# Optimization experiments

Hardware: AMD Instinct MI355X
Metric: run time of the kernel (lower is better)

Reference implementation:

```python
import jax, jax.numpy as jnp
import numpy as np

N, E, EMB, HID, FT, H = 2000, 32000, 768, 384, 768, 4
NEG_SLOPE = 0.2


def gat_conv(x, src, dst, edge_attr, W, a_src, a_dst, W_e, a_e, b):
    """PyG GATConv, concat=False (mean over heads), edge_dim, add_self_loops
    with fill_value='mean'. x:[N,Fin], edge_attr:[E,768]."""
    n = x.shape[0]
    h, c = a_src.shape
    # self loops: edge_attr of loop (i,i) = mean of incoming edge_attr at i
    deg = jax.ops.segment_sum(jnp.ones(src.shape[0], x.dtype), dst, num_segments=n)
    loop_attr = jax.ops.segment_sum(edge_attr, dst, num_segments=n) / jnp.maximum(deg, 1.0)[:, None]
    ar = jnp.arange(n)
    s = jnp.concatenate([src, ar])
    d = jnp.concatenate([dst, ar])
    ea = jnp.concatenate([edge_attr, loop_attr], axis=0)   # [E+N, 768]
    hx = (x @ W).reshape(n, h, c)                           # [N,H,C]
    he = (ea @ W_e).reshape(-1, h, c)                       # [E+N,H,C]
    alpha = (jnp.einsum('nhc,hc->nh', hx, a_src)[s]
             + jnp.einsum('nhc,hc->nh', hx, a_dst)[d]
             + jnp.einsum('ehc,hc->eh', he, a_e))           # [E+N,H]
    alpha = jax.nn.leaky_relu(alpha, NEG_SLOPE)
    # segment softmax over destination node (self loop guarantees nonempty)
    mx = jax.ops.segment_max(alpha, d, num_segments=n)
    ex = jnp.exp(alpha - mx[d])
    den = jax.ops.segment_sum(ex, d, num_segments=n)
    att = ex / den[d]                                       # [E+N,H]
    out = jax.ops.segment_sum(hx[s] * att[:, :, None], d, num_segments=n)  # [N,H,C]
    return out.mean(axis=1) + b


def setup_inputs() -> dict:
    key = jax.random.key(0)
    ks = jax.random.split(key, 16)
    w = lambda k, shape, s=0.05: (jax.random.normal(k, shape, jnp.float32) * s)
    return {
        'x': jax.random.randint(ks[0], (N, 2), 0, 178),
        'edge_index': jax.random.randint(ks[1], (2, E), 0, N),
        'edge_attr': jax.random.randint(ks[2], (E, 2), 0, 18),
        'x_emb': w(ks[3], (178, EMB)),
        'e_emb': w(ks[4], (18, EMB)),
        'W1': w(ks[5], (EMB, H * HID)),
        'as1': w(ks[6], (H, HID)),
        'ad1': w(ks[7], (H, HID)),
        'We1': w(ks[8], (EMB, H * HID)),
        'ae1': w(ks[9], (H, HID)),
        'b1': jnp.zeros((HID,), jnp.float32),
        'W2': w(ks[10], (HID, H * FT)),
        'as2': w(ks[11], (H, FT)),
        'ad2': w(ks[12], (H, FT)),
        'We2': w(ks[13], (EMB, H * FT)),
        'ae2': w(ks[14], (H, FT)),
        'b2': jnp.zeros((FT,), jnp.float32),
    }


def reference(x, edge_index, edge_attr, x_emb, e_emb, W1, as1, ad1, We1, ae1, b1,
              W2, as2, ad2, We2, ae2, b2):
    src, dst = edge_index[0], edge_index[1]
    xf = x_emb[x].sum(axis=1)          # [N,768]
    eaf = e_emb[edge_attr].sum(axis=1)  # [E,768]
    h = jax.nn.relu(gat_conv(xf, src, dst, eaf, W1, as1, ad1, We1, ae1, b1))
    out = gat_conv(h, src, dst, eaf, W2, as2, ad2, We2, ae2, b2)
    return out
```

## Files before the change

kernel.cpp:

```cpp
#include <hip/hip_runtime.h>
#include <hip/hip_bf16.h>

#define NN   2000
#define NE   32000
#define EMBD 768
#define NH   4
#define HID  384
#define NEG  0.2f
#define DCAP 128

#define GM 2000
#define GN 768
#define GK 1536
#define K1 768

typedef __bf16 bf16x8 __attribute__((ext_vector_type(8)));
typedef float  f32x4  __attribute__((ext_vector_type(4)));

__device__ inline float wsum(float v){
#pragma unroll
  for (int o = 32; o > 0; o >>= 1) v += __shfl_xor(v, o, 64);
  return v;
}
__device__ inline float wmax(float v){
#pragma unroll
  for (int o = 32; o > 0; o >>= 1) v = fmaxf(v, __shfl_xor(v, o, 64));
  return v;
}

__device__ inline unsigned short f2bf(float f){
  unsigned u = __float_as_uint(f);
  unsigned r = (u + 0x7FFFu + ((u >> 16) & 1u)) >> 16;
  return (unsigned short)r;
}
__device__ inline float bf2f(unsigned short h){
  return __uint_as_float(((unsigned)h) << 16);
}

__device__ inline void gload16(const void* g, void* l){
  __builtin_amdgcn_global_load_lds((const __attribute__((address_space(1))) void*)g,
                                   (__attribute__((address_space(3))) void*)l, 16, 0, 0);
}
__device__ inline float dot4(float4 a, float4 b){
  return a.x*b.x + a.y*b.y + a.z*b.z + a.w*b.w;
}

__global__ __launch_bounds__(1024) void k_cnt(const int* __restrict__ dst,
                                              int* __restrict__ offsets,
                                              int* __restrict__ cursor){
  __shared__ int cnt[NN];
  __shared__ int s[1024];
  int t = threadIdx.x;
  for (int i = t; i < NN; i += 1024) cnt[i] = 0;
  __syncthreads();
  for (int e = t; e < NE; e += 1024) atomicAdd(&cnt[dst[e]], 1);
  __syncthreads();
  int a = (2*t   < NN) ? cnt[2*t  ] : 0;
  int b = (2*t+1 < NN) ? cnt[2*t+1] : 0;
  s[t] = a + b;
  __syncthreads();
  for (int off = 1; off < 1024; off <<= 1){
    int v = (t >= off) ? s[t-off] : 0;
    __syncthreads();
    s[t] += v;
    __syncthreads();
  }
  int base = (t > 0) ? s[t-1] : 0;
  if (2*t < NN){ offsets[2*t] = base; cursor[2*t] = base; }
  if (2*t+1 < NN){ offsets[2*t+1] = base + a; cursor[2*t+1] = base + a; }
  if (2*t == NN) offsets[NN] = base;
}

__global__ __launch_bounds__(256) void k_prepA(
    const float* __restrict__ We1, const float* __restrict__ ae1,
    const float* __restrict__ W2,  const float* __restrict__ as2,
    const float* __restrict__ ad2, const float* __restrict__ We2,
    const float* __restrict__ ae2, const float* __restrict__ W1,
    const float* __restrict__ x_emb, const int* __restrict__ dst,
    float* __restrict__ we_a1, float* __restrict__ wa_s2,
    float* __restrict__ wa_d2, float* __restrict__ we_a2,
    unsigned short* __restrict__ Bh, unsigned short* __restrict__ Bl,
    unsigned short* __restrict__ W1th, unsigned short* __restrict__ W1tl,
    unsigned short* __restrict__ Xeh, unsigned short* __restrict__ Xel,
    int* __restrict__ cursor, int* __restrict__ csr){
  __shared__ __align__(16) float tile[64][65];
  int blk = blockIdx.x, t = threadIdx.x;
  if (blk < 384){
    int wid = blk*4 + (t >> 6);
    int lane = t & 63;
    bool lo32 = lane < 32;
    if (wid < 384){
      int kg = wid >> 2, h = wid & 3;
      int k0 = kg*8;
      const float4* ap = (const float4*)(ae1 + h*384);
      float4 a0 = ap[lane];
      float4 a1 = lo32 ? ap[64+lane] : make_float4(0,0,0,0);
      float res[8];
#pragma unroll
      for (int r = 0; r < 8; ++r){
        const float4* wr = (const float4*)(We1 + (size_t)(k0+r)*1536 + h*384);
        float s = dot4(wr[lane], a0);
        if (lo32) s += dot4(wr[64+lane], a1);
        res[r] = s;
      }
#pragma unroll
      for (int r = 0; r < 8; ++r) res[r] = wsum(res[r]);
      if (lane == 0){
#pragma unroll
        for (int r = 0; r < 8; ++r) we_a1[(k0+r)*4+h] = res[r];
      }
    } else if (wid < 768){
      int t2 = wid - 384;
      int kg = t2 >> 2, h = t2 & 3;
      int k0 = kg*4;
      const float4* s4 = (const float4*)(as2 + h*768);
      const float4* d4 = (const float4*)(ad2 + h*768);
      float4 sa[3], da[3];
#pragma unroll
      for (int i = 0; i < 3; ++i){ sa[i] = s4[i*64+lane]; da[i] = d4[i*64+lane]; }
      float r1[4], r2[4];
#pragma unroll
      for (int r = 0; r < 4; ++r){
        const float4* wr = (const float4*)(W2 + (size_t)(k0+r)*3072 + h*768);
        float s1 = 0.f, s2 = 0.f;
#pragma unroll
        for (int i = 0; i < 3; ++i){
          float4 w = wr[i*64+lane];
          s1 += dot4(w, sa[i]); s2 += dot4(w, da[i]);
        }
        r1[r] = s1; r2[r] = s2;
      }
#pragma unroll
      for (int r = 0; r < 4; ++r){ r1[r] = wsum(r1[r]); r2[r] = wsum(r2[r]); }
      if (lane == 0){
#pragma unroll
        for (int r = 0; r < 4; ++r){ wa_s2[(k0+r)*4+h] = r1[r]; wa_d2[(k0+r)*4+h] = r2[r]; }
      }
    } else {
      int t2 = wid - 768;
      int kg = t2 >> 2, h = t2 & 3;
      int k0 = kg*4;
      const float4* ap = (const float4*)(ae2 + h*768);
      float4 aa[3];
#pragma unroll
      for (int i = 0; i < 3; ++i) aa[i] = ap[i*64+lane];
      float res[4];
#pragma unroll
      for (int r = 0; r < 4; ++r){
        const float4* wr = (const float4*)(We2 + (size_t)(k0+r)*3072 + h*768);
        float s = 0.f;
#pragma unroll
        for (int i = 0; i < 3; ++i) s += dot4(wr[i*64+lane], aa[i]);
        res[r] = s;
      }
#pragma unroll
      for (int r = 0; r < 4; ++r) res[r] = wsum(res[r]);
      if (lane == 0){
#pragma unroll
        for (int r = 0; r < 4; ++r) we_a2[(k0+r)*4+h] = res[r];
      }
    }
  } else if (blk < 672){
    int idx = blk - 384;
    int bk = (idx % 24) * 64;
    int bc = (idx / 24) * 64;
    int cc = t & 63, kk4 = t >> 6;
#pragma unroll
    for (int i = 0; i < 16; ++i){
      int kk = kk4*16 + i;
      int k = bk + kk;
      int h = k / 384, kp = k - h*384;
      tile[kk][cc] = W2[(size_t)kp*3072 + h*768 + bc + cc];
    }
    __syncthreads();
    int kk2 = t & 63, cc4 = t >> 6;
#pragma unroll
    for (int i = 0; i < 16; ++i){
      int c2 = cc4*16 + i;
      float v = tile[kk2][c2];
      unsigned short hi = f2bf(v);
      unsigned short lo = f2bf(v - bf2f(hi));
      size_t o = (size_t)(bc + c2)*GK + bk + kk2;
      Bh[o] = hi; Bl[o] = lo;
    }
  } else if (blk < 960){
    int idx = blk - 672;
    int bkk = (idx % 12) * 64;
    int bcc = (idx / 12) * 64;
    int cc = t & 63, kk4 = t >> 6;
#pragma unroll
    for (int i = 0; i < 16; ++i){
      int kk = kk4*16 + i;
      tile[kk][cc] = W1[(size_t)(bkk+kk)*1536 + bcc + cc];
    }
    __syncthreads();
    int kk2 = t & 63, cc4 = t >> 6;
#pragma unroll
    for (int i = 0; i < 16; ++i){
      int c2 = cc4*16 + i;
      float v = tile[kk2][c2];
      unsigned short hi = f2bf(v);
      unsigned short lo = f2bf(v - bf2f(hi));
      size_t o = (size_t)(bcc + c2)*768 + bkk + kk2;
      W1th[o] = hi; W1tl[o] = lo;
    }
  } else if (blk < 1094){
    int i = (blk - 960)*256 + t;
    if (i < 34176){
      float4 v = ((const float4*)x_emb)[i];
      unsigned short h0 = f2bf(v.x), h1 = f2bf(v.y), h2 = f2bf(v.z), h3 = f2bf(v.w);
      ushort4 hh; hh.x = h0; hh.y = h1; hh.z = h2; hh.w = h3;
      ushort4 ll; ll.x = f2bf(v.x - bf2f(h0)); ll.y = f2bf(v.y - bf2f(h1));
      ll.z = f2bf(v.z - bf2f(h2)); ll.w = f2bf(v.w - bf2f(h3));
      ((ushort4*)Xeh)[i] = hh;
      ((ushort4*)Xel)[i] = ll;
    }
  } else {
    int e = (blk - 1094)*256 + t;
    if (e < NE){
      int pz = atomicAdd(&cursor[dst[e]], 1);
      csr[pz] = e;
    }
  }
}

__global__ __launch_bounds__(256) void k_mmX(const unsigned short* __restrict__ Ah,
                                             const unsigned short* __restrict__ Al,
                                             const unsigned short* __restrict__ Bh,
                                             const unsigned short* __restrict__ Bl,
                                             float* __restrict__ xh1){
  __shared__ __align__(16) unsigned short lds[2][4][64][64];
  int b = blockIdx.x;
  int bm = b / 24, bn = b % 24;
  int wave = threadIdx.x >> 6, lane = threadIdx.x & 63;
  int wm = wave >> 1, wn = wave & 1;
  int rl = lane & 15, kq = lane >> 4;

  int rt   = lane >> 3;
  int kswz = ((lane & 7) ^ rt) * 8;
  const unsigned short* sbase;
  int rowbase;
  if (wave == 0){ sbase = Ah; rowbase = bm*64; }
  else if (wave == 1){ sbase = Al; rowbase = bm*64; }
  else if (wave == 2){ sbase = Bh; rowbase = bn*64; }
  else { sbase = Bl; rowbase = bn*64; }
  bool isA = wave < 2;

  f32x4 acc[2][2] = {};

#pragma unroll
  for (int i = 0; i < 8; ++i){
    int row = rowbase + i*8 + rt;
    if (isA) row = (row < 178) ? row : 177;
    gload16(sbase + (size_t)row*768 + kswz, &lds[0][wave][i*8][0]);
  }
  __syncthreads();

  for (int t = 0; t < 12; ++t){
    int cur = t & 1;
    if (t < 11){
      int k0 = (t+1)*64;
#pragma unroll
      for (int i = 0; i < 8; ++i){
        int row = rowbase + i*8 + rt;
        if (isA) row = (row < 178) ? row : 177;
        gload16(sbase + (size_t)row*768 + k0 + kswz, &lds[cur^1][wave][i*8][0]);
      }
    }
#pragma unroll
    for (int ks = 0; ks < 2; ++ks){
      bf16x8 ah[2], al2[2], bh2[2], bl2[2];
#pragma unroll
      for (int i = 0; i < 2; ++i){
        int r = wm*32 + i*16 + rl;
        int sl = (ks*4 + kq) ^ (r & 7);
        ah[i]  = *(const bf16x8*)&lds[cur][0][r][sl*8];
        al2[i] = *(const bf16x8*)&lds[cur][1][r][sl*8];
      }
#pragma unroll
      for (int j = 0; j < 2; ++j){
        int cdx = wn*32 + j*16 + rl;
        int sl = (ks*4 + kq) ^ (cdx & 7);
        bh2[j] = *(const bf16x8*)&lds[cur][2][cdx][sl*8];
        bl2[j] = *(const bf16x8*)&lds[cur][3][cdx][sl*8];
      }
#pragma unroll
      for (int i = 0; i < 2; ++i){
#pragma unroll
        for (int j = 0; j < 2; ++j){
          acc[i][j] = __builtin_amdgcn_mfma_f32_16x16x32_bf16(ah[i],  bh2[j], acc[i][j], 0, 0, 0);
          acc[i][j] = __builtin_amdgcn_mfma_f32_16x16x32_bf16(ah[i],  bl2[j], acc[i][j], 0, 0, 0);
          acc[i][j] = __builtin_amdgcn_mfma_f32_16x16x32_bf16(al2[i], bh2[j], acc[i][j], 0, 0, 0);
        }
      }
    }
    __syncthreads();
  }

#pragma unroll
  for (int i = 0; i < 2; ++i){
#pragma unroll
    for (int j = 0; j < 2; ++j){
      int col = bn*64 + wn*32 + j*16 + rl;
#pragma unroll
      for (int r = 0; r < 4; ++r){
        int row = bm*64 + wm*32 + i*16 + kq*4 + r;
        if (row < 178) xh1[(size_t)row*1536 + col] = acc[i][j][r];
      }
    }
  }
}

__global__ __launch_bounds__(256) void k_prepB(
    const float* __restrict__ xh1,
    const float* __restrict__ as1, const float* __restrict__ ad1,
    const float* __restrict__ e_emb,
    const float* __restrict__ we_a1, const float* __restrict__ we_a2,
    unsigned short* __restrict__ XHh, unsigned short* __restrict__ XHl,
    float* __restrict__ xa_s1, float* __restrict__ xa_d1,
    float* __restrict__ ew1, float* __restrict__ ew2){
  int blk = blockIdx.x, t = threadIdx.x;
  if (blk < 178){
    int tok = blk;
    for (int i = t; i < 1536; i += 256){
      float v = xh1[(size_t)tok*1536 + i];
      int h = i / 384, c = i - h*384;
      size_t off = (size_t)c*K1 + h*192 + tok;
      unsigned short hi = f2bf(v);
      XHh[off] = hi; XHl[off] = f2bf(v - bf2f(hi));
    }
  } else if (blk < 356){
    int r = blk - 178;
    int h = t >> 6, lane = t & 63;
    const float4* p0 = (const float4*)(xh1 + (size_t)r*1536 + h*384);
    const float4* s4 = (const float4*)(as1 + h*384);
    const float4* d4 = (const float4*)(ad1 + h*384);
    float s1, s2;
    {
      float4 u = p0[lane], sa = s4[lane], da = d4[lane];
      s1 = dot4(u, sa); s2 = dot4(u, da);
    }
    if (lane < 32){
      float4 u = p0[64+lane], sa = s4[64+lane], da = d4[64+lane];
      s1 += dot4(u, sa); s2 += dot4(u, da);
    }
    s1 = wsum(s1); s2 = wsum(s2);
    if (lane == 0){ xa_s1[r*4+h] = s1; xa_d1[r*4+h] = s2; }
  } else if (blk < 392){
    int id = (blk - 356)*4 + (t >> 6);
    int lane = t & 63;
    const float* wv = (id < 72) ? we_a1 : we_a2;
    float* o = (id < 72) ? ew1 : ew2;
    int id2 = (id < 72) ? id : (id - 72);
    int r = id2 >> 2, h = id2 & 3;
    const float* ar = e_emb + (size_t)r*EMBD;
    float acc = 0.f;
    for (int k = lane; k < EMBD; k += 64) acc += ar[k] * wv[k*4+h];
    acc = wsum(acc);
    if (lane == 0) o[r*4+h] = acc;
  } else {
    int i = (blk - 392)*256 + t;
    if (i < 21504){
      int c = i / 56, rem = i - c*56;
      int h = rem / 14, tp = 178 + rem - h*14;
      size_t off = (size_t)c*K1 + h*192 + tp;
      XHh[off] = 0; XHl[off] = 0;
    }
  }
}

__global__ __launch_bounds__(256) void k_gat1sm(const int* __restrict__ offsets,
                      int* __restrict__ csr, const int* __restrict__ srcv,
                      const int* __restrict__ x, const int* __restrict__ ea,
                      const float* __restrict__ xa_s1, const float* __restrict__ xa_d1,
                      const float* __restrict__ ew1, float* __restrict__ spill,
                      unsigned short* __restrict__ Qh, unsigned short* __restrict__ Ql){
  __shared__ float wts[DCAP][5];
  __shared__ int   sE[DCAP];
  __shared__ int   sA[DCAP], sB[DCAP];
  __shared__ float coef[K1];
  int n = blockIdx.x, t = threadIdx.x;
  int w = t >> 6, lane = t & 63;
  int lo = offsets[n], hi = offsets[n+1];
  int deg = hi - lo;
  bool big = deg > DCAP;

  if (!big){
    if (deg <= 64){
      if (w == 0){
        int v = (lane < deg) ? csr[lo+lane] : 0x7fffffff;
#pragma unroll
        for (int k = 2; k <= 64; k <<= 1){
#pragma unroll
          for (int j2 = k >> 1; j2 > 0; j2 >>= 1){
            int o = __shfl_xor(v, j2, 64);
            bool lower = (lane & j2) == 0;
            bool asc   = (lane & k) == 0;
            v = (lower == asc) ? min(v, o) : max(v, o);
          }
        }
        sE[lane] = v;
        if (lane < deg) csr[lo+lane] = v;
      }
    } else {
      int m = 1; while (m < deg) m <<= 1;
      for (int i = t; i < m; i += 256) sE[i] = (i < deg) ? csr[lo+i] : 0x7fffffff;
      __syncthreads();
      for (int k = 2; k <= m; k <<= 1){
        for (int j2 = k >> 1; j2 > 0; j2 >>= 1){
          for (int i = t; i < m; i += 256){
            int ixj = i ^ j2;
            if (ixj > i){
              int a = sE[i], b = sE[ixj];
              bool up = ((i & k) == 0);
              if ((a > b) == up){ sE[i] = b; sE[ixj] = a; }
            }
          }
          __syncthreads();
        }
      }
      for (int i = t; i < deg; i += 256) csr[lo+i] = sE[i];
    }
  } else {
    if (t == 0){
      for (int i = lo+1; i < hi; ++i){
        int v = csr[i], j = i-1;
        while (j >= lo && csr[j] > v){ csr[j+1] = csr[j]; --j; }
        csr[j+1] = v;
      }
    }
  }
  for (int i = t; i < K1; i += 256) coef[i] = 0.f;
  __syncthreads();

  int xn0 = x[2*n], xn1 = x[2*n+1];
  float ad_n = xa_d1[xn0*4+w] + xa_d1[xn1*4+w];
  float as_n = xa_s1[xn0*4+w] + xa_s1[xn1*4+w];
  float mx = -3.4e38f, sae = 0.f;
  float wlv;
  if (!big){
    for (int j = lane; j < deg; j += 64){
      int e = sE[j]; int s = srcv[e];
      int a = x[2*s], b = x[2*s+1];
      if (w == 0){ sA[j] = a; sB[j] = b; }
      float ae = ew1[ea[2*e]*4+w] + ew1[ea[2*e+1]*4+w];
      float al = (xa_s1[a*4+w] + xa_s1[b*4+w]) + ad_n + ae;
      al = (al > 0.f) ? al : NEG * al;
      wts[j][w] = al;
      sae += ae; mx = fmaxf(mx, al);
    }
    mx = wmax(mx); sae = wsum(sae);
    float all_ = as_n + ad_n + sae / fmaxf((float)deg, 1.f);
    all_ = (all_ > 0.f) ? all_ : NEG * all_;
    mx = fmaxf(mx, all_);
    float den = 0.f;
    for (int j = lane; j < deg; j += 64){
      float xx = expf(wts[j][w] - mx);
      wts[j][w] = xx; den += xx;
    }
    den = wsum(den);
    float exl = expf(all_ - mx);
    den += exl;
    float inv = 1.f / den;
    for (int j = lane; j < deg; j += 64) wts[j][w] *= inv;
    wlv = exl * inv;
  } else {
    for (int p = lo + lane; p < hi; p += 64){
      int e = csr[p]; int s = srcv[e];
      int a = x[2*s], b = x[2*s+1];
      float ae = ew1[ea[2*e]*4+w] + ew1[ea[2*e+1]*4+w];
      float al = (xa_s1[a*4+w] + xa_s1[b*4+w]) + ad_n + ae;
      al = (al > 0.f) ? al : NEG * al;
      spill[e*4 + w] = al;
      sae += ae; mx = fmaxf(mx, al);
    }
    mx = wmax(mx); sae = wsum(sae);
    float all_ = as_n + ad_n + sae / fmaxf((float)deg, 1.f);
    all_ = (all_ > 0.f) ? all_ : NEG * all_;
    mx = fmaxf(mx, all_);
    float den = 0.f;
    for (int p = lo + lane; p < hi; p += 64){
      int e = csr[p];
      float xx = expf(spill[e*4 + w] - mx);
      spill[e*4 + w] = xx; den += xx;
    }
    den = wsum(den);
    float exl = expf(all_ - mx);
    den += exl;
    float inv = 1.f / den;
    for (int p = lo + lane; p < hi; p += 64) spill[csr[p]*4 + w] *= inv;
    wlv = exl * inv;
  }
  __syncthreads();

  if (lane == 0){
    float* cf = coef + w*192;
    if (!big){
      for (int j = 0; j < deg; ++j){
        float wj = wts[j][w];
        cf[sA[j]] += wj; cf[sB[j]] += wj;
      }
    } else {
      for (int p = lo; p < hi; ++p){
        int e = csr[p]; int s = srcv[e];
        float wj = spill[e*4 + w];
        cf[x[2*s]] += wj; cf[x[2*s+1]] += wj;
      }
    }
    cf[xn0] += wlv; cf[xn1] += wlv;
  }
  __syncthreads();

  for (int i = t; i < K1; i += 256){
    float v = coef[i];
    unsigned short hi16 = f2bf(v);
    Qh[(size_t)n*K1 + i] = hi16;
    Ql[(size_t)n*K1 + i] = f2bf(v - bf2f(hi16));
  }
}

__global__ __launch_bounds__(256) void k_mm1(const unsigned short* __restrict__ Qh,
                                             const unsigned short* __restrict__ Ql,
                                             const unsigned short* __restrict__ XHh,
                                             const unsigned short* __restrict__ XHl,
                                             const float* __restrict__ b1,
                                             float* __restrict__ hact){
  __shared__ __align__(16) unsigned short lds[2][4][64][64];
  int b = blockIdx.x;
  int xcd = b & 7, idx = b >> 3;
  int bm = xcd*4 + idx/6, bn = idx % 6;
  int wave = threadIdx.x >> 6, lane = threadIdx.x & 63;
  int wm = wave >> 1, wn = wave & 1;
  int rl = lane & 15, kq = lane >> 4;

  int rt   = lane >> 3;
  int kswz = ((lane & 7) ^ rt) * 8;
  const unsigned short* sbase;
  int rowbase;
  if (wave == 0){ sbase = Qh; rowbase = bm*64; }
  else if (wave == 1){ sbase = Ql; rowbase = bm*64; }
  else if (wave == 2){ sbase = XHh; rowbase = bn*64; }
  else { sbase = XHl; rowbase = bn*64; }
  bool isA = wave < 2;

  f32x4 acc[2][2] = {};

#pragma unroll
  for (int i = 0; i < 8; ++i){
    int row = rowbase + i*8 + rt;
    if (isA) row = (row < GM) ? row : (GM-1);
    gload16(sbase + (size_t)row*K1 + kswz, &lds[0][wave][i*8][0]);
  }
  __syncthreads();

  for (int t = 0; t < 12; ++t){
    int cur = t & 1;
    if (t < 11){
      int k0 = (t+1)*64;
#pragma unroll
      for (int i = 0; i < 8; ++i){
        int row = rowbase + i*8 + rt;
        if (isA) row = (row < GM) ? row : (GM-1);
        gload16(sbase + (size_t)row*K1 + k0 + kswz, &lds[cur^1][wave][i*8][0]);
      }
    }
#pragma unroll
    for (int ks = 0; ks < 2; ++ks){
      bf16x8 ah[2], al2[2], bh2[2], bl2[2];
#pragma unroll
      for (int i = 0; i < 2; ++i){
        int r = wm*32 + i*16 + rl;
        int sl = (ks*4 + kq) ^ (r & 7);
        ah[i]  = *(const bf16x8*)&lds[cur][0][r][sl*8];
        al2[i] = *(const bf16x8*)&lds[cur][1][r][sl*8];
      }
#pragma unroll
      for (int j = 0; j < 2; ++j){
        int cdx = wn*32 + j*16 + rl;
        int sl = (ks*4 + kq) ^ (cdx & 7);
        bh2[j] = *(const bf16x8*)&lds[cur][2][cdx][sl*8];
        bl2[j] = *(const bf16x8*)&lds[cur][3][cdx][sl*8];
      }
#pragma unroll
      for (int i = 0; i < 2; ++i){
#pragma unroll
        for (int j = 0; j < 2; ++j){
          acc[i][j] = __builtin_amdgcn_mfma_f32_16x16x32_bf16(ah[i],  bh2[j], acc[i][j], 0, 0, 0);
          acc[i][j] = __builtin_amdgcn_mfma_f32_16x16x32_bf16(ah[i],  bl2[j], acc[i][j], 0, 0, 0);
          acc[i][j] = __builtin_amdgcn_mfma_f32_16x16x32_bf16(al2[i], bh2[j], acc[i][j], 0, 0, 0);
        }
      }
    }
    __syncthreads();
  }

#pragma unroll
  for (int i = 0; i < 2; ++i){
#pragma unroll
    for (int j = 0; j < 2; ++j){
      int col = bn*64 + wn*32 + j*16 + rl;
      float bb = b1[col];
#pragma unroll
      for (int r = 0; r < 4; ++r){
        int row = bm*64 + wm*32 + i*16 + kq*4 + r;
        if (row < GM) hact[(size_t)row*HID + col] = fmaxf(0.25f*acc[i][j][r] + bb, 0.f);
      }
    }
  }
}

__global__ __launch_bounds__(256) void k_dots(const float* __restrict__ hact,
                      const float* __restrict__ wa_s2, const float* __restrict__ wa_d2,
                      float* __restrict__ asrc2, float* __restrict__ adst2){
  int w = threadIdx.x >> 6, lane = threadIdx.x & 63;
  int n = blockIdx.x*4 + w;
  float pr[8] = {};
#pragma unroll
  for (int i = 0; i < 6; ++i){
    int c = i*64 + lane;
    float v = hact[(size_t)n*HID + c];
#pragma unroll
    for (int h = 0; h < 4; ++h){
      pr[h]   += v * wa_s2[c*4+h];
      pr[4+h] += v * wa_d2[c*4+h];
    }
  }
#pragma unroll
  for (int o = 32; o > 0; o >>= 1){
#pragma unroll
    for (int q = 0; q < 8; ++q) pr[q] += __shfl_xor(pr[q], o, 64);
  }
  if (lane == 0){
#pragma unroll
    for (int h = 0; h < 4; ++h){ asrc2[n*4+h] = pr[h]; adst2[n*4+h] = pr[4+h]; }
  }
}

__global__ __launch_bounds__(384) void k_gat2(const int* __restrict__ offsets,
                      const int* __restrict__ csr, const int* __restrict__ srcv,
                      const int* __restrict__ ea,
                      const float* __restrict__ asrc, const float* __restrict__ adst,
                      const float* __restrict__ ew2,
                      const float* __restrict__ hact, float* __restrict__ spill,
                      unsigned short* __restrict__ Gh, unsigned short* __restrict__ Gl){
  __shared__ float wts[DCAP][5];
  __shared__ int   ssrc[DCAP];
  __shared__ float wl[4];
  int n = blockIdx.x, t = threadIdx.x;
  int w = t >> 6, lane = t & 63;
  int lo = offsets[n], hi = offsets[n+1];
  int deg = hi - lo;
  bool big = deg > DCAP;
  if (w < 4){
    float ad_n = adst[n*NH + w];
    float as_n = asrc[n*NH + w];
    float mx = -3.4e38f, sae = 0.f;
    if (!big){
      for (int p = lo + lane; p < hi; p += 64){
        int e = csr[p]; int s = srcv[e];
        if (w == 0) ssrc[p - lo] = s;
        float ae = ew2[ea[2*e]*4+w] + ew2[ea[2*e+1]*4+w];
        float al = asrc[s*NH + w] + ad_n + ae;
        al = (al > 0.f) ? al : NEG * al;
        wts[p - lo][w] = al;
        sae += ae; mx = fmaxf(mx, al);
      }
      mx = wmax(mx); sae = wsum(sae);
      float all_ = as_n + ad_n + sae / fmaxf((float)deg, 1.f);
      all_ = (all_ > 0.f) ? all_ : NEG * all_;
      mx = fmaxf(mx, all_);
      float den = 0.f;
      for (int p = lo + lane; p < hi; p += 64){
        float xx = expf(wts[p - lo][w] - mx);
        wts[p - lo][w] = xx; den += xx;
      }
      den = wsum(den);
      float exl = expf(all_ - mx);
      den += exl;
      float inv = 1.f / den;
      for (int p = lo + lane; p < hi; p += 64) wts[p - lo][w] *= inv;
      if (lane == 0) wl[w] = exl * inv;
    } else {
      for (int p = lo + lane; p < hi; p += 64){
        int e = csr[p];
        float ae = ew2[ea[2*e]*4+w] + ew2[ea[2*e+1]*4+w];
        float al = asrc[srcv[e]*NH + w] + ad_n + ae;
        al = (al > 0.f) ? al : NEG * al;
        spill[e*4 + w] = al;
        sae += ae; mx = fmaxf(mx, al);
      }
      mx = wmax(mx); sae = wsum(sae);
      float all_ = as_n + ad_n + sae / fmaxf((float)deg, 1.f);
      all_ = (all_ > 0.f) ? all_ : NEG * all_;
      mx = fmaxf(mx, all_);
      float den = 0.f;
      for (int p = lo + lane; p < hi; p += 64){
        int e = csr[p];
        float xx = expf(spill[e*4 + w] - mx);
        spill[e*4 + w] = xx; den += xx;
      }
      den = wsum(den);
      float exl = expf(all_ - mx);
      den += exl;
      float inv = 1.f / den;
      for (int p = lo + lane; p < hi; p += 64) spill[csr[p]*4 + w] *= inv;
      if (lane == 0) wl[w] = exl * inv;
    }
  }
  __syncthreads();

  int c = t;
  float a0 = 0.f, a1 = 0.f, a2 = 0.f, a3 = 0.f;
  if (!big){
    float vnext = 0.f;
    if (deg > 0) vnext = hact[(size_t)ssrc[0]*HID + c];
    for (int j = 0; j < deg; ++j){
      float vc = vnext;
      if (j+1 < deg) vnext = hact[(size_t)ssrc[j+1]*HID + c];
      float w0=wts[j][0], w1=wts[j][1], w2=wts[j][2], w3=wts[j][3];
      a0 += w0*vc; a1 += w1*vc; a2 += w2*vc; a3 += w3*vc;
    }
  } else {
    for (int j = 0; j < deg; ++j){
      int e = csr[lo+j]; int s = srcv[e];
      float w0 = spill[e*4+0], w1 = spill[e*4+1], w2 = spill[e*4+2], w3 = spill[e*4+3];
      float vc = hact[(size_t)s*HID + c];
      a0 += w0*vc; a1 += w1*vc; a2 += w2*vc; a3 += w3*vc;
    }
  }
  {
    float vc = hact[(size_t)n*HID + c];
    a0 += wl[0]*vc; a1 += wl[1]*vc; a2 += wl[2]*vc; a3 += wl[3]*vc;
  }
  size_t base = (size_t)n*GK + c;
  float vv[4] = {a0, a1, a2, a3};
#pragma unroll
  for (int h = 0; h < 4; ++h){
    unsigned short hi16 = f2bf(vv[h]);
    unsigned short lo16 = f2bf(vv[h] - bf2f(hi16));
    Gh[base + h*384] = hi16;
    Gl[base + h*384] = lo16;
  }
}

__global__ __launch_bounds__(256) void k_mm2(const unsigned short* __restrict__ Gh,
                                             const unsigned short* __restrict__ Gl,
                                             const unsigned short* __restrict__ Bh,
                                             const unsigned short* __restrict__ Bl,
                                             const float* __restrict__ b2,
                                             float* __restrict__ out){
  __shared__ __align__(16) unsigned short lds[2][4][64][64];
  int b = blockIdx.x;
  int xcd = b & 7, idx = b >> 3;
  int bm = xcd*4 + idx/12, bn = idx % 12;
  int wave = threadIdx.x >> 6, lane = threadIdx.x & 63;
  int wm = wave >> 1, wn = wave & 1;
  int rl = lane & 15, kq = lane >> 4;

  int rt   = lane >> 3;
  int kswz = ((lane & 7) ^ rt) * 8;
  const unsigned short* sbase;
  int rowbase;
  if (wave == 0){ sbase = Gh; rowbase = bm*64; }
  else if (wave == 1){ sbase = Gl; rowbase = bm*64; }
  else if (wave == 2){ sbase = Bh; rowbase = bn*64; }
  else { sbase = Bl; rowbase = bn*64; }
  bool isA = wave < 2;

  f32x4 acc[2][2] = {};

#pragma unroll
  for (int i = 0; i < 8; ++i){
    int row = rowbase + i*8 + rt;
    if (isA) row = (row < GM) ? row : (GM-1);
    gload16(sbase + (size_t)row*GK + kswz, &lds[0][wave][i*8][0]);
  }
  __syncthreads();

  for (int t = 0; t < 24; ++t){
    int cur = t & 1;
    if (t < 23){
      int k0 = (t+1)*64;
#pragma unroll
      for (int i = 0; i < 8; ++i){
        int row = rowbase + i*8 + rt;
        if (isA) row = (row < GM) ? row : (GM-1);
        gload16(sbase + (size_t)row*GK + k0 + kswz, &lds[cur^1][wave][i*8][0]);
      }
    }
#pragma unroll
    for (int ks = 0; ks < 2; ++ks){
      bf16x8 ah[2], al2[2], bh2[2], bl2[2];
#pragma unroll
      for (int i = 0; i < 2; ++i){
        int r = wm*32 + i*16 + rl;
        int sl = (ks*4 + kq) ^ (r & 7);
        ah[i]  = *(const bf16x8*)&lds[cur][0][r][sl*8];
        al2[i] = *(const bf16x8*)&lds[cur][1][r][sl*8];
      }
#pragma unroll
      for (int j = 0; j < 2; ++j){
        int cdx = wn*32 + j*16 + rl;
        int sl = (ks*4 + kq) ^ (cdx & 7);
        bh2[j] = *(const bf16x8*)&lds[cur][2][cdx][sl*8];
        bl2[j] = *(const bf16x8*)&lds[cur][3][cdx][sl*8];
      }
#pragma unroll
      for (int i = 0; i < 2; ++i){
#pragma unroll
        for (int j = 0; j < 2; ++j){
          acc[i][j] = __builtin_amdgcn_mfma_f32_16x16x32_bf16(ah[i],  bh2[j], acc[i][j], 0, 0, 0);
          acc[i][j] = __builtin_amdgcn_mfma_f32_16x16x32_bf16(ah[i],  bl2[j], acc[i][j], 0, 0, 0);
          acc[i][j] = __builtin_amdgcn_mfma_f32_16x16x32_bf16(al2[i], bh2[j], acc[i][j], 0, 0, 0);
        }
      }
    }
    __syncthreads();
  }

#pragma unroll
  for (int i = 0; i < 2; ++i){
#pragma unroll
    for (int j = 0; j < 2; ++j){
      int col = bn*64 + wn*32 + j*16 + rl;
      float bb = b2[col];
#pragma unroll
      for (int r = 0; r < 4; ++r){
        int row = bm*64 + wm*32 + i*16 + kq*4 + r;
        if (row < GM) out[(size_t)row*GN + col] = 0.25f*acc[i][j][r] + bb;
      }
    }
  }
}

extern "C" void kernel_launch(void* const* d_in, const int* in_sizes, int n_in,
                              void* d_out, int out_size, void* d_ws, size_t ws_size,
                              hipStream_t stream){
  const int*   x     = (const int*)d_in[0];
  const int*   ei    = (const int*)d_in[1];
  const int*   ea    = (const int*)d_in[2];
  const float* x_emb = (const float*)d_in[3];
  const float* e_emb = (const float*)d_in[4];
  const float* W1    = (const float*)d_in[5];
  const float* as1   = (const float*)d_in[6];
  const float* ad1   = (const float*)d_in[7];
  const float* We1   = (const float*)d_in[8];
  const float* ae1   = (const float*)d_in[9];
  const float* b1    = (const float*)d_in[10];
  const float* W2    = (const float*)d_in[11];
  const float* as2   = (const float*)d_in[12];
  const float* ad2   = (const float*)d_in[13];
  const float* We2   = (const float*)d_in[14];
  const float* ae2   = (const float*)d_in[15];
  const float* b2    = (const float*)d_in[16];
  const int* srcv = ei;
  const int* dstv = ei + NE;
  float* out = (float*)d_out;

  char* p = (char*)d_ws;
  auto take = [&](size_t n){ void* q = (void*)p; p += (n + 255) & ~(size_t)255; return q; };
  int*   cursor  = (int*)take(NN*4);
  int*   offsets = (int*)take((NN+1)*4);
  int*   csr     = (int*)take(NE*4);
  float* we_a1   = (float*)take(EMBD*NH*4);
  float* wa_s2   = (float*)take(HID*NH*4);
  float* wa_d2   = (float*)take(HID*NH*4);
  float* we_a2   = (float*)take(EMBD*NH*4);
  float* xa_s1   = (float*)take(178*NH*4);
  float* xa_d1   = (float*)take(178*NH*4);
  float* ew1     = (float*)take(18*NH*4);
  float* ew2     = (float*)take(18*NH*4);
  float* xh1     = (float*)take((size_t)178*1536*4);
  unsigned short* Xeh  = (unsigned short*)take((size_t)178*768*2);
  unsigned short* Xel  = (unsigned short*)take((size_t)178*768*2);
  unsigned short* W1th = (unsigned short*)take((size_t)1536*768*2);
  unsigned short* W1tl = (unsigned short*)take((size_t)1536*768*2);
  unsigned short* XHh  = (unsigned short*)take((size_t)HID*K1*2);
  unsigned short* XHl  = (unsigned short*)take((size_t)HID*K1*2);
  unsigned short* Qh   = (unsigned short*)take((size_t)NN*K1*2);
  unsigned short* Ql   = (unsigned short*)take((size_t)NN*K1*2);
  unsigned short* Bth  = (unsigned short*)take((size_t)GN*GK*2);
  unsigned short* Btl  = (unsigned short*)take((size_t)GN*GK*2);
  unsigned short* Gh   = (unsigned short*)take((size_t)GM*GK*2);
  unsigned short* Gl   = (unsigned short*)take((size_t)GM*GK*2);
  float* spill   = (float*)take((size_t)NE*NH*4);
  float* hact    = (float*)take((size_t)NN*HID*4);
  float* asrc2   = (float*)take(NN*NH*4);
  float* adst2   = (float*)take(NN*NH*4);

  k_cnt<<<1, 1024, 0, stream>>>(dstv, offsets, cursor);

  k_prepA<<<1219, 256, 0, stream>>>(We1, ae1, W2, as2, ad2, We2, ae2, W1,
                                    x_emb, dstv, we_a1, wa_s2, wa_d2, we_a2,
                                    Bth, Btl, W1th, W1tl, Xeh, Xel,
                                    cursor, csr);
  k_mmX<<<72, 256, 0, stream>>>(Xeh, Xel, W1th, W1tl, xh1);
  k_prepB<<<476, 256, 0, stream>>>(xh1, as1, ad1, e_emb, we_a1, we_a2,
                                   XHh, XHl, xa_s1, xa_d1, ew1, ew2);

  k_gat1sm<<<NN, 256, 0, stream>>>(offsets, csr, srcv, x, ea, xa_s1, xa_d1,
                                   ew1, spill, Qh, Ql);
  k_mm1<<<192, 256, 0, stream>>>(Qh, Ql, XHh, XHl, b1, hact);
  k_dots<<<500, 256, 0, stream>>>(hact, wa_s2, wa_d2, asrc2, adst2);

  k_gat2<<<NN, 384, 0, stream>>>(offsets, csr, srcv, ea, asrc2, adst2, ew2,
                                 hact, spill, Gh, Gl);

  k_mm2<<<384, 256, 0, stream>>>(Gh, Gl, Bth, Btl, b2, out);
}
```

Baseline: 117.0 us.

## Fold prepB into mmX by precomputing W1·a_src/a_dst and writing split bf16 directly

Precomputes W1 projected onto the layer-1 attention vectors (wa_s1, wa_d1) in the prep kernel, so per-token attention logits come straight from x_emb instead of from the intermediate xh1. The x_emb-by-W1 GEMM now writes the hi/lo bf16 transposed XH layout in its epilogue, and the zero-padding and edge-embedding dot work moves into the prep and mmX launches. This drops the fp32 xh1 buffer and one kernel launch with its global round trip. The reassociation changes the fp32 rounding order of the attention logits slightly.

```diff
diff --git a/kernel.cpp b/kernel.cpp
--- a/kernel.cpp
+++ b/kernel.cpp
@@ -76,12 +76,15 @@
     const float* __restrict__ W2,  const float* __restrict__ as2,
     const float* __restrict__ ad2, const float* __restrict__ We2,
     const float* __restrict__ ae2, const float* __restrict__ W1,
+    const float* __restrict__ as1, const float* __restrict__ ad1,
     const float* __restrict__ x_emb, const int* __restrict__ dst,
     float* __restrict__ we_a1, float* __restrict__ wa_s2,
     float* __restrict__ wa_d2, float* __restrict__ we_a2,
+    float* __restrict__ wa_s1, float* __restrict__ wa_d1,
     unsigned short* __restrict__ Bh, unsigned short* __restrict__ Bl,
     unsigned short* __restrict__ W1th, unsigned short* __restrict__ W1tl,
     unsigned short* __restrict__ Xeh, unsigned short* __restrict__ Xel,
+    unsigned short* __restrict__ XHh, unsigned short* __restrict__ XHl,
     int* __restrict__ cursor, int* __restrict__ csr){
   __shared__ __align__(16) float tile[64][65];
   int blk = blockIdx.x, t = threadIdx.x;
@@ -160,8 +163,42 @@
         for (int r = 0; r < 4; ++r) we_a2[(k0+r)*4+h] = res[r];
       }
     }
-  } else if (blk < 672){
-    int idx = blk - 384;
+  } else if (blk < 480){
+    int wid = (blk-384)*4 + (t >> 6);
+    int lane = t & 63;
+    bool lo32 = lane < 32;
+    int kg = wid >> 2, h = wid & 3;
+    int k0 = kg*8;
+    const float4* sp = (const float4*)(as1 + h*384);
+    const float4* dp = (const float4*)(ad1 + h*384);
+    float4 sa0 = sp[lane];
+    float4 sa1 = lo32 ? sp[64+lane] : make_float4(0,0,0,0);
+    float4 da0 = dp[lane];
+    float4 da1 = lo32 ? dp[64+lane] : make_float4(0,0,0,0);
+    float r1[8], r2[8];
+#pragma unroll
+    for (int r = 0; r < 8; ++r){
+      const float4* wr = (const float4*)(W1 + (size_t)(k0+r)*1536 + h*384);
+      float4 w0 = wr[lane];
+      float s1 = dot4(w0, sa0);
+      float s2 = dot4(w0, da0);
+      if (lo32){
+        float4 w1 = wr[64+lane];
+        s1 += dot4(w1, sa1); s2 += dot4(w1, da1);
+      }
+      r1[r] = s1; r2[r] = s2;
+    }
+#pragma unroll
+    for (int r = 0; r < 8; ++r){ r1[r] = wsum(r1[r]); r2[r] = wsum(r2[r]); }
+    if (lane == 0){
+#pragma unroll
+      for (int r = 0; r < 8; ++r){
+        wa_s1[h*768 + k0 + r] = r1[r];
+        wa_d1[h*768 + k0 + r] = r2[r];
+      }
+    }
+  } else if (blk < 768){
+    int idx = blk - 480;
     int bk = (idx % 24) * 64;
     int bc = (idx / 24) * 64;
     int cc = t & 63, kk4 = t >> 6;
@@ -183,8 +220,8 @@
       size_t o = (size_t)(bc + c2)*GK + bk + kk2;
       Bh[o] = hi; Bl[o] = lo;
     }
-  } else if (blk < 960){
-    int idx = blk - 672;
+  } else if (blk < 1056){
+    int idx = blk - 768;
     int bkk = (idx % 12) * 64;
     int bcc = (idx / 12) * 64;
     int cc = t & 63, kk4 = t >> 6;
@@ -204,8 +241,8 @@
       size_t o = (size_t)(bcc + c2)*768 + bkk + kk2;
       W1th[o] = hi; W1tl[o] = lo;
     }
-  } else if (blk < 1094){
-    int i = (blk - 960)*256 + t;
+  } else if (blk < 1190){
+    int i = (blk - 1056)*256 + t;
     if (i < 34176){
       float4 v = ((const float4*)x_emb)[i];
       unsigned short h0 = f2bf(v.x), h1 = f2bf(v.y), h2 = f2bf(v.z), h3 = f2bf(v.w);
@@ -215,8 +252,16 @@
       ((ushort4*)Xeh)[i] = hh;
       ((ushort4*)Xel)[i] = ll;
     }
+  } else if (blk < 1274){
+    int i = (blk - 1190)*256 + t;
+    if (i < 21504){
+      int c = i / 56, rem = i - c*56;
+      int h = rem / 14, tp = 178 + rem - h*14;
+      size_t off = (size_t)c*K1 + h*192 + tp;
+      XHh[off] = 0; XHl[off] = 0;
+    }
   } else {
-    int e = (blk - 1094)*256 + t;
+    int e = (blk - 1274)*256 + t;
     if (e < NE){
       int pz = atomicAdd(&cursor[dst[e]], 1);
       csr[pz] = e;
@@ -228,127 +273,125 @@
                                              const unsigned short* __restrict__ Al,
                                              const unsigned short* __restrict__ Bh,
                                              const unsigned short* __restrict__ Bl,
-                                             float* __restrict__ xh1){
+                                             const float* __restrict__ x_emb,
+                                             const float* __restrict__ e_emb,
+                                             const float* __restrict__ wa_s1,
+                                             const float* __restrict__ wa_d1,
+                                             const float* __restrict__ we_a1,
+                                             const float* __restrict__ we_a2,
+                                             unsigned short* __restrict__ XHh,
+                                             unsigned short* __restrict__ XHl,
+                                             float* __restrict__ xa_s1,
+                                             float* __restrict__ xa_d1,
+                                             float* __restrict__ ew1,
+                                             float* __restrict__ ew2){
   __shared__ __align__(16) unsigned short lds[2][4][64][64];
-  int b = blockIdx.x;
-  int bm = b / 24, bn = b % 24;
-  int wave = threadIdx.x >> 6, lane = threadIdx.x & 63;
-  int wm = wave >> 1, wn = wave & 1;
-  int rl = lane & 15, kq = lane >> 4;
-
-  int rt   = lane >> 3;
-  int kswz = ((lane & 7) ^ rt) * 8;
-  const unsigned short* sbase;
-  int rowbase;
-  if (wave == 0){ sbase = Ah; rowbase = bm*64; }
-  else if (wave == 1){ sbase = Al; rowbase = bm*64; }
-  else if (wave == 2){ sbase = Bh; rowbase = bn*64; }
-  else { sbase = Bl; rowbase = bn*64; }
-  bool isA = wave < 2;
-
-  f32x4 acc[2][2] = {};
-
-#pragma unroll
-  for (int i = 0; i < 8; ++i){
-    int row = rowbase + i*8 + rt;
-    if (isA) row = (row < 178) ? row : 177;
-    gload16(sbase + (size_t)row*768 + kswz, &lds[0][wave][i*8][0]);
-  }
-  __syncthreads();
-
-  for (int t = 0; t < 12; ++t){
-    int cur = t & 1;
-    if (t < 11){
-      int k0 = (t+1)*64;
-#pragma unroll
-      for (int i = 0; i < 8; ++i){
-        int row = rowbase + i*8 + rt;
-        if (isA) row = (row < 178) ? row : 177;
-        gload16(sbase + (size_t)row*768 + k0 + kswz, &lds[cur^1][wave][i*8][0]);
-      }
-    }
-#pragma unroll
-    for (int ks = 0; ks < 2; ++ks){
-      bf16x8 ah[2], al2[2], bh2[2], bl2[2];
-#pragma unroll
-      for (int i = 0; i < 2; ++i){
-        int r = wm*32 + i*16 + rl;
-        int sl = (ks*4 + kq) ^ (r & 7);
-        ah[i]  = *(const bf16x8*)&lds[cur][0][r][sl*8];
-        al2[i] = *(const bf16x8*)&lds[cur][1][r][sl*8];
-      }
+  int blk = blockIdx.x;
+  if (blk < 72){
+    int b = blk;
+    int bm = b / 24, bn = b % 24;
+    int wave = threadIdx.x >> 6, lane = threadIdx.x & 63;
+    int wm = wave >> 1, wn = wave & 1;
+    int rl = lane & 15, kq = lane >> 4;
+
+    int rt   = lane >> 3;
+    int kswz = ((lane & 7) ^ rt) * 8;
+    const unsigned short* sbase;
+    int rowbase;
+    if (wave == 0){ sbase = Ah; rowbase = bm*64; }
+    else if (wave == 1){ sbase = Al; rowbase = bm*64; }
+    else if (wave == 2){ sbase = Bh; rowbase = bn*64; }
+    else { sbase = Bl; rowbase = bn*64; }
+    bool isA = wave < 2;
+
+    f32x4 acc[2][2] = {};
+
+#pragma unroll
+    for (int i = 0; i < 8; ++i){
+      int row = rowbase + i*8 + rt;
+      if (isA) row = (row < 178) ? row : 177;
+      gload16(sbase + (size_t)row*768 + kswz, &lds[0][wave][i*8][0]);
+    }
+    __syncthreads();
+
+    for (int t = 0; t < 12; ++t){
+      int cur = t & 1;
+      if (t < 11){
+        int k0 = (t+1)*64;
+#pragma unroll
+        for (int i = 0; i < 8; ++i){
+          int row = rowbase + i*8 + rt;
+          if (isA) row = (row < 178) ? row : 177;
+          gload16(sbase + (size_t)row*768 + k0 + kswz, &lds[cur^1][wave][i*8][0]);
+        }
+      }
+#pragma unroll
+      for (int ks = 0; ks < 2; ++ks){
+        bf16x8 ah[2], al2[2], bh2[2], bl2[2];
+#pragma unroll
+        for (int i = 0; i < 2; ++i){
+          int r = wm*32 + i*16 + rl;
+          int sl = (ks*4 + kq) ^ (r & 7);
+          ah[i]  = *(const bf16x8*)&lds[cur][0][r][sl*8];
+          al2[i] = *(const bf16x8*)&lds[cur][1][r][sl*8];
+        }
+#pragma unroll
+        for (int j = 0; j < 2; ++j){
+          int cdx = wn*32 + j*16 + rl;
+          int sl = (ks*4 + kq) ^ (cdx & 7);
+          bh2[j] = *(const bf16x8*)&lds[cur][2][cdx][sl*8];
+          bl2[j] = *(const bf16x8*)&lds[cur][3][cdx][sl*8];
+        }
+#pragma unroll
+        for (int i = 0; i < 2; ++i){
+#pragma unroll
+          for (int j = 0; j < 2; ++j){
+            acc[i][j] = __builtin_amdgcn_mfma_f32_16x16x32_bf16(ah[i],  bh2[j], acc[i][j], 0, 0, 0);
+            acc[i][j] = __builtin_amdgcn_mfma_f32_16x16x32_bf16(ah[i],  bl2[j], acc[i][j], 0, 0, 0);
+            acc[i][j] = __builtin_amdgcn_mfma_f32_16x16x32_bf16(al2[i], bh2[j], acc[i][j], 0, 0, 0);
+          }
+        }
+      }
+      __syncthreads();
+    }
+
+#pragma unroll
+    for (int i = 0; i < 2; ++i){
 #pragma unroll
       for (int j = 0; j < 2; ++j){
-        int cdx = wn*32 + j*16 + rl;
-        int sl = (ks*4 + kq) ^ (cdx & 7);
-        bh2[j] = *(const bf16x8*)&lds[cur][2][cdx][sl*8];
-        bl2[j] = *(const bf16x8*)&lds[cur][3][cdx][sl*8];
-      }
-#pragma unroll
-      for (int i = 0; i < 2; ++i){
-#pragma unroll
-        for (int j = 0; j < 2; ++j){
-          acc[i][j] = __builtin_amdgcn_mfma_f32_16x16x32_bf16(ah[i],  bh2[j], acc[i][j], 0, 0, 0);
-          acc[i][j] = __builtin_amdgcn_mfma_f32_16x16x32_bf16(ah[i],  bl2[j], acc[i][j], 0, 0, 0);
-          acc[i][j] = __builtin_amdgcn_mfma_f32_16x16x32_bf16(al2[i], bh2[j], acc[i][j], 0, 0, 0);
+        int col = bn*64 + wn*32 + j*16 + rl;
+        int h = col / 384, c = col - h*384;
+        size_t cb = (size_t)c*K1 + h*192;
+#pragma unroll
+        for (int r = 0; r < 4; ++r){
+          int row = bm*64 + wm*32 + i*16 + kq*4 + r;
+          if (row < 178){
+            float v = acc[i][j][r];
+            unsigned short hi = f2bf(v);
+            XHh[cb + row] = hi;
+            XHl[cb + row] = f2bf(v - bf2f(hi));
+          }
         }
       }
     }
-    __syncthreads();
-  }
-
-#pragma unroll
-  for (int i = 0; i < 2; ++i){
-#pragma unroll
-    for (int j = 0; j < 2; ++j){
-      int col = bn*64 + wn*32 + j*16 + rl;
-#pragma unroll
-      for (int r = 0; r < 4; ++r){
-        int row = bm*64 + wm*32 + i*16 + kq*4 + r;
-        if (row < 178) xh1[(size_t)row*1536 + col] = acc[i][j][r];
-      }
-    }
-  }
-}
-
-__global__ __launch_bounds__(256) void k_prepB(
-    const float* __restrict__ xh1,
-    const float* __restrict__ as1, const float* __restrict__ ad1,
-    const float* __restrict__ e_emb,
-    const float* __restrict__ we_a1, const float* __restrict__ we_a2,
-    unsigned short* __restrict__ XHh, unsigned short* __restrict__ XHl,
-    float* __restrict__ xa_s1, float* __restrict__ xa_d1,
-    float* __restrict__ ew1, float* __restrict__ ew2){
-  int blk = blockIdx.x, t = threadIdx.x;
-  if (blk < 178){
-    int tok = blk;
-    for (int i = t; i < 1536; i += 256){
-      float v = xh1[(size_t)tok*1536 + i];
-      int h = i / 384, c = i - h*384;
-      size_t off = (size_t)c*K1 + h*192 + tok;
-      unsigned short hi = f2bf(v);
-      XHh[off] = hi; XHl[off] = f2bf(v - bf2f(hi));
-    }
-  } else if (blk < 356){
-    int r = blk - 178;
-    int h = t >> 6, lane = t & 63;
-    const float4* p0 = (const float4*)(xh1 + (size_t)r*1536 + h*384);
-    const float4* s4 = (const float4*)(as1 + h*384);
-    const float4* d4 = (const float4*)(ad1 + h*384);
-    float s1, s2;
-    {
-      float4 u = p0[lane], sa = s4[lane], da = d4[lane];
-      s1 = dot4(u, sa); s2 = dot4(u, da);
-    }
-    if (lane < 32){
-      float4 u = p0[64+lane], sa = s4[64+lane], da = d4[64+lane];
-      s1 += dot4(u, sa); s2 += dot4(u, da);
+  } else if (blk < 250){
+    int r = blk - 72;
+    int h = threadIdx.x >> 6, lane = threadIdx.x & 63;
+    const float4* xe = (const float4*)(x_emb + (size_t)r*768);
+    const float4* ws = (const float4*)(wa_s1 + h*768);
+    const float4* wd = (const float4*)(wa_d1 + h*768);
+    float s1 = 0.f, s2 = 0.f;
+#pragma unroll
+    for (int i = 0; i < 3; ++i){
+      float4 u = xe[i*64+lane];
+      s1 += dot4(u, ws[i*64+lane]);
+      s2 += dot4(u, wd[i*64+lane]);
     }
     s1 = wsum(s1); s2 = wsum(s2);
     if (lane == 0){ xa_s1[r*4+h] = s1; xa_d1[r*4+h] = s2; }
-  } else if (blk < 392){
-    int id = (blk - 356)*4 + (t >> 6);
-    int lane = t & 63;
+  } else {
+    int id = (blk - 250)*4 + (threadIdx.x >> 6);
+    int lane = threadIdx.x & 63;
     const float* wv = (id < 72) ? we_a1 : we_a2;
     float* o = (id < 72) ? ew1 : ew2;
     int id2 = (id < 72) ? id : (id - 72);
@@ -358,14 +401,6 @@
     for (int k = lane; k < EMBD; k += 64) acc += ar[k] * wv[k*4+h];
     acc = wsum(acc);
     if (lane == 0) o[r*4+h] = acc;
-  } else {
-    int i = (blk - 392)*256 + t;
-    if (i < 21504){
-      int c = i / 56, rem = i - c*56;
-      int h = rem / 14, tp = 178 + rem - h*14;
-      size_t off = (size_t)c*K1 + h*192 + tp;
-      XHh[off] = 0; XHl[off] = 0;
-    }
   }
 }
 
@@ -866,11 +901,12 @@
   float* wa_s2   = (float*)take(HID*NH*4);
   float* wa_d2   = (float*)take(HID*NH*4);
   float* we_a2   = (float*)take(EMBD*NH*4);
+  float* wa_s1   = (float*)take(NH*EMBD*4);
+  float* wa_d1   = (float*)take(NH*EMBD*4);
   float* xa_s1   = (float*)take(178*NH*4);
   float* xa_d1   = (float*)take(178*NH*4);
   float* ew1     = (float*)take(18*NH*4);
   float* ew2     = (float*)take(18*NH*4);
-  float* xh1     = (float*)take((size_t)178*1536*4);
   unsigned short* Xeh  = (unsigned short*)take((size_t)178*768*2);
   unsigned short* Xel  = (unsigned short*)take((size_t)178*768*2);
   unsigned short* W1th = (unsigned short*)take((size_t)1536*768*2);
@@ -890,13 +926,15 @@
 
   k_cnt<<<1, 1024, 0, stream>>>(dstv, offsets, cursor);
 
-  k_prepA<<<1219, 256, 0, stream>>>(We1, ae1, W2, as2, ad2, We2, ae2, W1,
-                                    x_emb, dstv, we_a1, wa_s2, wa_d2, we_a2,
+  k_prepA<<<1399, 256, 0, stream>>>(We1, ae1, W2, as2, ad2, We2, ae2, W1,
+                                    as1, ad1, x_emb, dstv,
+                                    we_a1, wa_s2, wa_d2, we_a2, wa_s1, wa_d1,
                                     Bth, Btl, W1th, W1tl, Xeh, Xel,
-                                    cursor, csr);
-  k_mmX<<<72, 256, 0, stream>>>(Xeh, Xel, W1th, W1tl, xh1);
-  k_prepB<<<476, 256, 0, stream>>>(xh1, as1, ad1, e_emb, we_a1, we_a2,
-                                   XHh, XHl, xa_s1, xa_d1, ew1, ew2);
+                                    XHh, XHl, cursor, csr);
+
+  k_mmX<<<286, 256, 0, stream>>>(Xeh, Xel, W1th, W1tl, x_emb, e_emb,
+                                 wa_s1, wa_d1, we_a1, we_a2,
+                                 XHh, XHl, xa_s1, xa_d1, ew1, ew2);
 
   k_gat1sm<<<NN, 256, 0, stream>>>(offsets, csr, srcv, x, ea, xa_s1, xa_d1,
                                    ew1, spill, Qh, Ql);
```

Result: faster. 112.2 us, median of 2 (-4.1%).
